# Optimization experiments

Hardware: AMD Instinct MI355X
Metric: run time of the kernel (lower is better)

The kernel has to match this reference:

```python
import jax, jax.numpy as jnp
import numpy as np

B, N, D, H = 2, 2048, 1024, 16
HD = D // H  # head dim = 64
SCALING = (D / H) ** 0.5  # sqrt(64) = 8
EPS = 1e-5


def setup_inputs() -> dict:
    key = jax.random.key(0)
    k1, k2, k3 = jax.random.split(key, 3)
    return {
        "z": jax.random.normal(k1, (B, N, D), dtype=jnp.float32),
        "ln_scale": jnp.ones((D,), dtype=jnp.float32),
        "ln_bias": jnp.zeros((D,), dtype=jnp.float32),
        "w_qkv": jax.random.normal(k2, (D, 3 * D), dtype=jnp.float32) * (D ** -0.5),
        "w_proj": jax.random.normal(k3, (D, D), dtype=jnp.float32) * (D ** -0.5),
        "b_proj": jnp.zeros((D,), dtype=jnp.float32),
    }


def reference(z, ln_scale, ln_bias, w_qkv, w_proj, b_proj):
    b, n, d = z.shape
    # LayerNorm (pre-norm)
    mu = jnp.mean(z, axis=-1, keepdims=True)
    var = jnp.mean(jnp.square(z - mu), axis=-1, keepdims=True)
    zn = (z - mu) / jnp.sqrt(var + EPS) * ln_scale + ln_bias
    # QKV projection: [b, n, 3D]
    qkv = zn @ w_qkv
    # einops 'b n (h d qkv_n) -> qkv_n b h n d': qkv index is innermost
    qkv5 = qkv.reshape(b, n, H, HD, 3)  # [b, n, h, d, 3]
    q = jnp.transpose(qkv5[..., 0], (0, 2, 1, 3))  # [b, h, n, d]
    k = jnp.transpose(qkv5[..., 1], (0, 2, 1, 3))
    v = jnp.transpose(qkv5[..., 2], (0, 2, 1, 3))
    # Attention: scores scaled AFTER the matmul, as in the source
    scores = jnp.einsum('bhqd,bhkd->bhqk', q, k) / SCALING
    att = jax.nn.softmax(scores, axis=-1)
    out = jnp.einsum('bhal,bhlv->bhav', att, v)  # [b, h, n, d]
    out = jnp.transpose(out, (0, 2, 1, 3)).reshape(b, n, d)  # merge heads
    out = out @ w_proj + b_proj  # projection (dropout p=0)
    return z + out
```

## Files before the change

kernel.cpp:

```cpp
#include <hip/hip_runtime.h>
#include <stdint.h>
#include <math.h>

typedef unsigned short u16;
typedef float f32x4 __attribute__((ext_vector_type(4)));
typedef __bf16 bf16x8 __attribute__((ext_vector_type(8)));

__device__ __forceinline__ u16 f2bf(float f) {
    union { float f; uint32_t u; } c; c.f = f;
    return (u16)((c.u + 0x7FFFu + ((c.u >> 16) & 1u)) >> 16);
}

__device__ __forceinline__ void gload_lds16(const void* g, void* l) {
    __builtin_amdgcn_global_load_lds(
        (const __attribute__((address_space(1))) unsigned int*)g,
        (__attribute__((address_space(3))) unsigned int*)l, 16, 0, 0);
}

__global__ __launch_bounds__(256) void prep_kernel(const float* __restrict__ z,
                                                   const float* __restrict__ sc,
                                                   const float* __restrict__ bs,
                                                   const float* __restrict__ w_qkv,
                                                   const float* __restrict__ w_proj,
                                                   u16* __restrict__ zn,
                                                   u16* __restrict__ wqkvT,
                                                   u16* __restrict__ wprojT) {
    __shared__ float t[32][33];
    const int tid = threadIdx.x;
    const int bid = blockIdx.x;

    if (bid < 4096) {
        float* red = &t[0][0];
        const int row = bid;
        const float4 v = ((const float4*)(z + (size_t)row * 1024))[tid];
        float s = v.x + v.y + v.z + v.w;
        #pragma unroll
        for (int off = 32; off > 0; off >>= 1) s += __shfl_xor(s, off);
        if ((tid & 63) == 0) red[tid >> 6] = s;
        __syncthreads();
        const float mean = (red[0] + red[1] + red[2] + red[3]) * (1.0f / 1024.0f);
        const float dx = v.x - mean, dy = v.y - mean, dz = v.z - mean, dw = v.w - mean;
        float q = dx * dx + dy * dy + dz * dz + dw * dw;
        #pragma unroll
        for (int off = 32; off > 0; off >>= 1) q += __shfl_xor(q, off);
        if ((tid & 63) == 0) red[4 + (tid >> 6)] = q;
        __syncthreads();
        const float var = (red[4] + red[5] + red[6] + red[7]) * (1.0f / 1024.0f);
        const float rstd = rsqrtf(var + 1e-5f);
        const float4 scv = ((const float4*)sc)[tid];
        const float4 bsv = ((const float4*)bs)[tid];
        const u16 o0 = f2bf(dx * rstd * scv.x + bsv.x);
        const u16 o1 = f2bf(dy * rstd * scv.y + bsv.y);
        const u16 o2 = f2bf(dz * rstd * scv.z + bsv.z);
        const u16 o3 = f2bf(dw * rstd * scv.w + bsv.w);
        uint2 pk;
        pk.x = (uint32_t)o0 | ((uint32_t)o1 << 16);
        pk.y = (uint32_t)o2 | ((uint32_t)o3 << 16);
        *(uint2*)&zn[(size_t)row * 1024 + tid * 4] = pk;
        return;
    }

    const float* in;
    u16* out;
    int K, N, permute, bx, by;
    if (bid < 4096 + 3072) {
        const int r = bid - 4096;
        in = w_qkv; out = wqkvT; K = 1024; N = 3072; permute = 1;
        bx = r % 96; by = r / 96;
    } else {
        const int r = bid - 4096 - 3072;
        in = w_proj; out = wprojT; K = 1024; N = 1024; permute = 0;
        bx = r % 32; by = r / 32;
    }
    const int j = tid & 31, i0 = tid >> 5;
    const int kb = by * 32, nb = bx * 32;
    #pragma unroll
    for (int p = 0; p < 4; ++p) {
        int r = i0 + p * 8;
        t[r][j] = in[(size_t)(kb + r) * N + nb + j];
    }
    __syncthreads();
    #pragma unroll
    for (int p = 0; p < 4; ++p) {
        int r = i0 + p * 8;
        int c = nb + r;
        int np = c;
        if (permute) {
            int h = c / 192, rem = c - h * 192;
            int d = rem / 3, s = rem - d * 3;
            np = s * 1024 + h * 64 + d;
        }
        out[(size_t)np * K + kb + j] = f2bf(t[j][r]);
    }
}

__global__ __launch_bounds__(256, 3) void gemm_qkv(const u16* __restrict__ A,
                                                   const u16* __restrict__ Bt,
                                                   u16* __restrict__ qbuf,
                                                   u16* __restrict__ kbuf,
                                                   u16* __restrict__ vT) {
    __shared__ __align__(16) u16 sm[64 * 136];
    u16* const As = sm;
    u16* const Bs = sm + 4096;
    const int tid = threadIdx.x;
    const int wave = tid >> 6, lane = tid & 63;
    const int quad = lane >> 4, l16 = lane & 15;
    const int wm = (wave >> 1) * 64, wn = (wave & 1) * 64;
    const int row0 = blockIdx.x * 128, col0 = blockIdx.y * 128;
    const int gr = lane >> 2, gc = (lane & 3) * 8;
    f32x4 acc[4][4] = {};
    for (int kt = 0; kt < 1024; kt += 32) {
        __syncthreads();
        #pragma unroll
        for (int i = 0; i < 2; ++i) {
            const int rb = wave * 16 + i * 64;
            gload_lds16(&A[(size_t)(row0 + rb + gr) * 1024 + kt + gc], &As[rb * 32]);
            gload_lds16(&Bt[(size_t)(col0 + rb + gr) * 1024 + kt + gc], &Bs[rb * 32]);
        }
        __syncthreads();
        bf16x8 ax[4], bx[4];
        #pragma unroll
        for (int t = 0; t < 4; ++t) {
            ax[t] = *(const bf16x8*)&As[(wm + t * 16 + l16) * 32 + quad * 8];
            bx[t] = *(const bf16x8*)&Bs[(wn + t * 16 + l16) * 32 + quad * 8];
        }
        #pragma unroll
        for (int mt = 0; mt < 4; ++mt)
            #pragma unroll
            for (int nt = 0; nt < 4; ++nt)
                acc[mt][nt] = __builtin_amdgcn_mfma_f32_16x16x32_bf16(ax[mt], bx[nt], acc[mt][nt], 0, 0, 0);
    }
    const int s = col0 >> 10;
    if (s < 2) {
        u16* const dst = (s == 0) ? qbuf : kbuf;
        const float scl = (s == 0) ? 0.125f * 1.44269504088896f : 1.0f;
        #pragma unroll
        for (int mt = 0; mt < 4; ++mt) {
            #pragma unroll
            for (int nt = 0; nt < 4; ++nt) {
                #pragma unroll
                for (int e = 0; e < 4; ++e) {
                    const int row = row0 + wm + mt * 16 + quad * 4 + e;
                    const int col = col0 + wn + nt * 16 + l16;
                    const int b = row >> 11, n = row & 2047;
                    const int h = (col >> 6) & 15, d = col & 63;
                    dst[((size_t)(b * 16 + h) * 2048 + n) * 64 + d] = f2bf(acc[mt][nt][e] * scl);
                }
            }
        }
    } else {
        const int b = row0 >> 11, n0 = row0 & 2047;
        const int h0 = (col0 >> 6) & 15;
        for (int hh = 0; hh < 2; ++hh) {
            __syncthreads();
            if ((wave & 1) == hh) {
                #pragma unroll
                for (int mt = 0; mt < 4; ++mt) {
                    const int rl = wm + mt * 16 + quad * 4;
                    #pragma unroll
                    for (int nt = 0; nt < 4; ++nt) {
                        const int cl = nt * 16 + l16;
                        u16 tmp[4];
                        #pragma unroll
                        for (int e = 0; e < 4; ++e) tmp[e] = f2bf(acc[mt][nt][e]);
                        *(uint2*)&sm[cl * 136 + rl] = *(const uint2*)tmp;
                    }
                }
            }
            __syncthreads();
            const int bh = b * 16 + h0 + hh;
            #pragma unroll
            for (int pass = 0; pass < 4; ++pass) {
                const int chunk = pass * 256 + tid;
                const int d = chunk >> 4;
                const int nc = chunk & 15;
                const uint4 vv = *(const uint4*)&sm[d * 136 + nc * 8];
                *(uint4*)&vT[((size_t)bh * 64 + d) * 2048 + n0 + nc * 8] = vv;
            }
        }
    }
}

__global__ __launch_bounds__(256, 2) void attn_kernel(const u16* __restrict__ qb,
                                                      const u16* __restrict__ kb,
                                                      const u16* __restrict__ vT,
                                                      u16* __restrict__ att_out) {
    __shared__ __align__(16) u16 smem[2][16384];
    const int tid = threadIdx.x;
    const int wave = tid >> 6, lane = tid & 63;
    const int quad = lane >> 4, l16 = lane & 15;
    const int qt = blockIdx.x, bh = blockIdx.y;
    const int b = bh >> 4, h = bh & 15;

    const u16* qrowA = &qb[(size_t)(bh * 2048 + qt * 128 + wave * 32 + l16) * 64];
    const bf16x8 qA0 = *(const bf16x8*)&qrowA[quad * 8];
    const bf16x8 qA1 = *(const bf16x8*)&qrowA[32 + quad * 8];
    const u16* qrowB = qrowA + 16 * 64;
    const bf16x8 qB0 = *(const bf16x8*)&qrowB[quad * 8];
    const bf16x8 qB1 = *(const bf16x8*)&qrowB[32 + quad * 8];

    const u16* ksrc[4];
    const u16* vsrc[4];
    int kofs[4], vofs[4];
    #pragma unroll
    for (int j = 0; j < 4; ++j) {
        const int p = 8 * wave + 32 * j + (lane >> 3);
        const int kr = (p & 0x60) | ((p & 12) << 1) | ((p & 16) >> 2) | (p & 3);
        const int gk = (lane & 7) ^ (p & 7);
        ksrc[j] = kb + ((size_t)bh * 2048 + kr) * 64 + gk * 8;
        kofs[j] = (8 * wave + 32 * j) * 64;
        const int d = 4 * wave + 16 * j + (lane >> 4);
        const int gv = (lane & 15) ^ (d & 15);
        vsrc[j] = vT + ((size_t)bh * 64 + d) * 2048 + gv * 8;
        vofs[j] = 8192 + (4 * wave + 16 * j) * 128;
    }

    f32x4 oA[4] = {}, oB[4] = {};
    f32x4 lA = {}, lB = {};
    bf16x8 ones;
    #pragma unroll
    for (int i = 0; i < 8; ++i) ones[i] = (__bf16)1.0f;

    #pragma unroll
    for (int j = 0; j < 4; ++j) {
        gload_lds16(ksrc[j], &smem[0][kofs[j]]);
        gload_lds16(vsrc[j], &smem[0][vofs[j]]);
        ksrc[j] += 128 * 64;
        vsrc[j] += 128;
    }

    for (int kt = 0; kt < 16; ++kt) {
        __syncthreads();
        if (kt < 15) {
            u16* nb_ = smem[(kt + 1) & 1];
            #pragma unroll
            for (int j = 0; j < 4; ++j) {
                gload_lds16(ksrc[j], &nb_[kofs[j]]);
                gload_lds16(vsrc[j], &nb_[vofs[j]]);
                ksrc[j] += 128 * 64;
                vsrc[j] += 128;
            }
        }
        const u16* Ks = smem[kt & 1];
        const u16* Vs = smem[kt & 1] + 8192;

        f32x4 sA[8] = {}, sB[8] = {};
        __builtin_amdgcn_s_setprio(1);
        #pragma unroll
        for (int nt = 0; nt < 8; ++nt) {
            const int r = nt * 16 + l16;
            const bf16x8 k0 = *(const bf16x8*)&Ks[r * 64 + (((quad) ^ (r & 7)) << 3)];
            const bf16x8 k1 = *(const bf16x8*)&Ks[r * 64 + (((quad + 4) ^ (r & 7)) << 3)];
            sA[nt] = __builtin_amdgcn_mfma_f32_16x16x32_bf16(k0, qA0, sA[nt], 0, 0, 0);
            sA[nt] = __builtin_amdgcn_mfma_f32_16x16x32_bf16(k1, qA1, sA[nt], 0, 0, 0);
            sB[nt] = __builtin_amdgcn_mfma_f32_16x16x32_bf16(k0, qB0, sB[nt], 0, 0, 0);
            sB[nt] = __builtin_amdgcn_mfma_f32_16x16x32_bf16(k1, qB1, sB[nt], 0, 0, 0);
        }
        __builtin_amdgcn_s_setprio(0);

        bf16x8 apA[4], apB[4];
        #pragma unroll
        for (int nt = 0; nt < 8; ++nt) {
            #pragma unroll
            for (int e = 0; e < 4; ++e) {
                apA[nt >> 1][(nt & 1) * 4 + e] = (__bf16)__builtin_amdgcn_exp2f(sA[nt][e]);
                apB[nt >> 1][(nt & 1) * 4 + e] = (__bf16)__builtin_amdgcn_exp2f(sB[nt][e]);
            }
        }

        __builtin_amdgcn_s_setprio(1);
        #pragma unroll
        for (int vt = 0; vt < 4; ++vt) {
            const int dd = vt * 16 + l16;
            #pragma unroll
            for (int c = 0; c < 4; ++c) {
                const bf16x8 vf = *(const bf16x8*)&Vs[dd * 128 + (((c * 4 + quad) ^ l16) << 3)];
                oA[vt] = __builtin_amdgcn_mfma_f32_16x16x32_bf16(apA[c], vf, oA[vt], 0, 0, 0);
                oB[vt] = __builtin_amdgcn_mfma_f32_16x16x32_bf16(apB[c], vf, oB[vt], 0, 0, 0);
            }
        }
        #pragma unroll
        for (int c = 0; c < 4; ++c) {
            lA = __builtin_amdgcn_mfma_f32_16x16x32_bf16(apA[c], ones, lA, 0, 0, 0);
            lB = __builtin_amdgcn_mfma_f32_16x16x32_bf16(apB[c], ones, lB, 0, 0, 0);
        }
        __builtin_amdgcn_s_setprio(0);
    }

    #pragma unroll
    for (int e = 0; e < 4; ++e) {
        const float invA = 1.0f / lA[e];
        const float invB = 1.0f / lB[e];
        const int nA = qt * 128 + wave * 32 + quad * 4 + e;
        #pragma unroll
        for (int vt = 0; vt < 4; ++vt) {
            att_out[(size_t)(b * 2048 + nA) * 1024 + h * 64 + vt * 16 + l16] = f2bf(oA[vt][e] * invA);
            att_out[(size_t)(b * 2048 + nA + 16) * 1024 + h * 64 + vt * 16 + l16] = f2bf(oB[vt][e] * invB);
        }
    }
}

__global__ __launch_bounds__(256, 3) void gemm_proj(const u16* __restrict__ A,
                                                    const u16* __restrict__ Bt,
                                                    const float* __restrict__ bias,
                                                    const float* __restrict__ z,
                                                    float* __restrict__ out) {
    __shared__ __align__(16) u16 sm[2 * 4096];
    u16* const As = sm;
    u16* const Bs = sm + 4096;
    const int tid = threadIdx.x;
    const int wave = tid >> 6, lane = tid & 63;
    const int quad = lane >> 4, l16 = lane & 15;
    const int wm = (wave >> 1) * 64, wn = (wave & 1) * 64;
    const int row0 = blockIdx.x * 128, col0 = blockIdx.y * 128;
    const int gr = lane >> 2, gc = (lane & 3) * 8;
    f32x4 acc[4][4] = {};
    for (int kt = 0; kt < 1024; kt += 32) {
        __syncthreads();
        #pragma unroll
        for (int i = 0; i < 2; ++i) {
            const int rb = wave * 16 + i * 64;
            gload_lds16(&A[(size_t)(row0 + rb + gr) * 1024 + kt + gc], &As[rb * 32]);
            gload_lds16(&Bt[(size_t)(col0 + rb + gr) * 1024 + kt + gc], &Bs[rb * 32]);
        }
        __syncthreads();
        bf16x8 ax[4], bx[4];
        #pragma unroll
        for (int t = 0; t < 4; ++t) {
            ax[t] = *(const bf16x8*)&As[(wm + t * 16 + l16) * 32 + quad * 8];
            bx[t] = *(const bf16x8*)&Bs[(wn + t * 16 + l16) * 32 + quad * 8];
        }
        #pragma unroll
        for (int mt = 0; mt < 4; ++mt)
            #pragma unroll
            for (int nt = 0; nt < 4; ++nt)
                acc[mt][nt] = __builtin_amdgcn_mfma_f32_16x16x32_bf16(ax[mt], bx[nt], acc[mt][nt], 0, 0, 0);
    }
    #pragma unroll
    for (int mt = 0; mt < 4; ++mt) {
        #pragma unroll
        for (int nt = 0; nt < 4; ++nt) {
            #pragma unroll
            for (int e = 0; e < 4; ++e) {
                const int row = row0 + wm + mt * 16 + quad * 4 + e;
                const int col = col0 + wn + nt * 16 + l16;
                out[(size_t)row * 1024 + col] = acc[mt][nt][e] + bias[col] + z[(size_t)row * 1024 + col];
            }
        }
    }
}

extern "C" void kernel_launch(void* const* d_in, const int* in_sizes, int n_in,
                              void* d_out, int out_size, void* d_ws, size_t ws_size,
                              hipStream_t stream) {
    const float* z        = (const float*)d_in[0];
    const float* ln_scale = (const float*)d_in[1];
    const float* ln_bias  = (const float*)d_in[2];
    const float* w_qkv    = (const float*)d_in[3];
    const float* w_proj   = (const float*)d_in[4];
    const float* b_proj   = (const float*)d_in[5];
    float* out = (float*)d_out;

    char* ws = (char*)d_ws;
    u16* zn     = (u16*)(ws);
    u16* wqkvT  = (u16*)(ws + (8u << 20));
    u16* wprojT = (u16*)(ws + (14u << 20));
    u16* qbuf   = (u16*)(ws + (16u << 20));
    u16* kbuf   = (u16*)(ws + (24u << 20));
    u16* vT     = (u16*)(ws + (32u << 20));
    u16* att_o  = (u16*)(ws + (40u << 20));

    prep_kernel<<<dim3(4096 + 3072 + 1024), 256, 0, stream>>>(
        z, ln_scale, ln_bias, w_qkv, w_proj, zn, wqkvT, wprojT);
    gemm_qkv<<<dim3(32, 24), 256, 0, stream>>>(zn, wqkvT, qbuf, kbuf, vT);
    attn_kernel<<<dim3(16, 32), 256, 0, stream>>>(qbuf, kbuf, vT, att_o);
    gemm_proj<<<dim3(32, 8), 256, 0, stream>>>(att_o, wprojT, b_proj, z, out);
}
```

Baseline: 176.0 us.

## Vectorize weight transpose in prep and remap block order for XCD locality

The weight transpose/convert path now handles 32x64 tiles per block, using float4 global loads and writing packed 8×bf16 (uint4) stores instead of scalar element accesses, which halves the transpose block count. In addition, the GEMM and attention kernels remap the linear block id with a stride-8 swizzle so blocks that share operand tiles land on the same XCD, aiming to improve L2 reuse. The remap assumes round-robin dispatch across 8 XCDs, and the LDS reads in the transpose may have bank conflicts.

```diff
diff --git a/kernel.cpp b/kernel.cpp
--- a/kernel.cpp
+++ b/kernel.cpp
@@ -25,7 +25,7 @@
                                                    u16* __restrict__ zn,
                                                    u16* __restrict__ wqkvT,
                                                    u16* __restrict__ wprojT) {
-    __shared__ float t[32][33];
+    __shared__ __align__(16) float t[32][68];
     const int tid = threadIdx.x;
     const int bid = blockIdx.x;
 
@@ -62,36 +62,36 @@
 
     const float* in;
     u16* out;
-    int K, N, permute, bx, by;
-    if (bid < 4096 + 3072) {
+    int N, permute, bx, by;
+    if (bid < 4096 + 1536) {
         const int r = bid - 4096;
-        in = w_qkv; out = wqkvT; K = 1024; N = 3072; permute = 1;
-        bx = r % 96; by = r / 96;
+        in = w_qkv; out = wqkvT; N = 3072; permute = 1;
+        bx = r % 48; by = r / 48;
     } else {
-        const int r = bid - 4096 - 3072;
-        in = w_proj; out = wprojT; K = 1024; N = 1024; permute = 0;
-        bx = r % 32; by = r / 32;
-    }
-    const int j = tid & 31, i0 = tid >> 5;
-    const int kb = by * 32, nb = bx * 32;
-    #pragma unroll
-    for (int p = 0; p < 4; ++p) {
-        int r = i0 + p * 8;
-        t[r][j] = in[(size_t)(kb + r) * N + nb + j];
-    }
+        const int r = bid - 4096 - 1536;
+        in = w_proj; out = wprojT; N = 1024; permute = 0;
+        bx = r % 16; by = r / 16;
+    }
+    const int kb = by * 32, nb = bx * 64;
+    const int lr = tid >> 3, lq = tid & 7;
+    const float* src = &in[(size_t)(kb + lr) * N + nb + lq * 8];
+    const float4 va = *(const float4*)src;
+    const float4 vb = *(const float4*)(src + 4);
+    *(float4*)&t[lr][lq * 8] = va;
+    *(float4*)&t[lr][lq * 8 + 4] = vb;
     __syncthreads();
-    #pragma unroll
-    for (int p = 0; p < 4; ++p) {
-        int r = i0 + p * 8;
-        int c = nb + r;
-        int np = c;
-        if (permute) {
-            int h = c / 192, rem = c - h * 192;
-            int d = rem / 3, s = rem - d * 3;
-            np = s * 1024 + h * 64 + d;
-        }
-        out[(size_t)np * K + kb + j] = f2bf(t[j][r]);
-    }
+    const int cj = tid >> 6, c = tid & 63;
+    const int col = nb + c;
+    int np = col;
+    if (permute) {
+        const int h = col / 192, rem = col - h * 192;
+        const int d = rem / 3, s = rem - d * 3;
+        np = s * 1024 + h * 64 + d;
+    }
+    u16 pk[8];
+    #pragma unroll
+    for (int u = 0; u < 8; ++u) pk[u] = f2bf(t[cj * 8 + u][c]);
+    *(uint4*)&out[(size_t)np * 1024 + kb + cj * 8] = *(const uint4*)pk;
 }
 
 __global__ __launch_bounds__(256, 3) void gemm_qkv(const u16* __restrict__ A,
@@ -106,7 +106,10 @@
     const int wave = tid >> 6, lane = tid & 63;
     const int quad = lane >> 4, l16 = lane & 15;
     const int wm = (wave >> 1) * 64, wn = (wave & 1) * 64;
-    const int row0 = blockIdx.x * 128, col0 = blockIdx.y * 128;
+    const int lin = blockIdx.y * 32 + blockIdx.x;
+    const int nlin = (lin & 7) * 96 + (lin >> 3);
+    const int bxs = nlin & 31, bys = nlin >> 5;
+    const int row0 = bxs * 128, col0 = bys * 128;
     const int gr = lane >> 2, gc = (lane & 3) * 8;
     f32x4 acc[4][4] = {};
     for (int kt = 0; kt < 1024; kt += 32) {
@@ -189,7 +192,9 @@
     const int tid = threadIdx.x;
     const int wave = tid >> 6, lane = tid & 63;
     const int quad = lane >> 4, l16 = lane & 15;
-    const int qt = blockIdx.x, bh = blockIdx.y;
+    const int lin = blockIdx.y * 16 + blockIdx.x;
+    const int nlin = (lin & 7) * 64 + (lin >> 3);
+    const int qt = nlin & 15, bh = nlin >> 4;
     const int b = bh >> 4, h = bh & 15;
 
     const u16* qrowA = &qb[(size_t)(bh * 2048 + qt * 128 + wave * 32 + l16) * 64];
@@ -312,7 +317,10 @@
     const int wave = tid >> 6, lane = tid & 63;
     const int quad = lane >> 4, l16 = lane & 15;
     const int wm = (wave >> 1) * 64, wn = (wave & 1) * 64;
-    const int row0 = blockIdx.x * 128, col0 = blockIdx.y * 128;
+    const int lin = blockIdx.y * 32 + blockIdx.x;
+    const int nlin = (lin & 7) * 32 + (lin >> 3);
+    const int bxs = nlin & 31, bys = nlin >> 5;
+    const int row0 = bxs * 128, col0 = bys * 128;
     const int gr = lane >> 2, gc = (lane & 3) * 8;
     f32x4 acc[4][4] = {};
     for (int kt = 0; kt < 1024; kt += 32) {
@@ -370,7 +378,7 @@
     u16* vT     = (u16*)(ws + (32u << 20));
     u16* att_o  = (u16*)(ws + (40u << 20));
 
-    prep_kernel<<<dim3(4096 + 3072 + 1024), 256, 0, stream>>>(
+    prep_kernel<<<dim3(4096 + 1536 + 512), 256, 0, stream>>>(
         z, ln_scale, ln_bias, w_qkv, w_proj, zn, wqkvT, wprojT);
     gemm_qkv<<<dim3(32, 24), 256, 0, stream>>>(zn, wqkvT, qbuf, kbuf, vT);
     attn_kernel<<<dim3(16, 32), 256, 0, stream>>>(qbuf, kbuf, vT, att_o);
```

Result: no change. 177.3 us (+0.7%).
